# Kernel tuning notes

Hardware: AMD Instinct MI355X
Metric: run time of the kernel (lower is better)

## Reference

```python
import jax, jax.numpy as jnp
import numpy as np

DIM = 1024
HID = 2048
E = 8
K = 2
EPS = 1e-9


def setup_inputs() -> dict:
    key = jax.random.key(0)
    ks = jax.random.split(key, 6)
    scale = 0.02
    return {
        "x": jax.random.normal(ks[0], (4, 2048, DIM), jnp.float32),
        "gate_w": jax.random.normal(ks[1], (DIM, E), jnp.float32) * scale,
        "gate_b": jnp.zeros((E,), jnp.float32),
        # stacked expert weights: leading dim = expert index
        "w1": jax.random.normal(ks[2], (E, DIM, HID), jnp.float32) * scale,
        "b1": jnp.zeros((E, HID), jnp.float32),
        "w2": jax.random.normal(ks[3], (E, DIM, HID), jnp.float32) * scale,
        "b2": jnp.zeros((E, HID), jnp.float32),
        "w3": jax.random.normal(ks[4], (E, HID, DIM), jnp.float32) * scale,
        "b3": jnp.zeros((E, DIM), jnp.float32),
    }


def reference(x, gate_w, gate_b, w1, b1, w2, b2, w3, b3):
    # x: (b, s, d)
    logits = x @ gate_w + gate_b                      # (b, s, E)
    scores = jax.nn.softmax(logits, axis=-1)
    topk_scores, topk_idx = jax.lax.top_k(scores, K)  # (b, s, K)

    usage = scores.mean(axis=(0, 1))                  # (E,)
    load_balance_loss = jnp.sum(usage * jnp.log(usage + EPS))

    # per-expert combine weight: score if expert in top-k else 0  -> (b, s, E)
    onehot = jax.nn.one_hot(topk_idx, E, dtype=x.dtype)            # (b, s, K, E)
    combine = jnp.sum(topk_scores[..., None] * onehot, axis=2)     # (b, s, E)

    out = jnp.zeros_like(x)
    for e in range(E):  # small fixed loop over experts
        gate = jax.nn.sigmoid(x @ w2[e] + b2[e])      # (b, s, H)
        h = (x @ w1[e] + b1[e]) * gate                # SwiGLU hidden
        out = out + combine[..., e:e + 1] * (h @ w3[e] + b3[e])
    return out, load_balance_loss
```

## Files before the change

### kernel.cpp

```cpp
#include <hip/hip_runtime.h>
#include <hip/hip_bf16.h>
#include <math.h>

#define N_TOK 8192
#define DIM   1024
#define HID   2048
#define NE    8
#define NT1   16
#define NT2   32
#define NB1   16
#define NB2   4
#define MAXT  72
#define PANEL1_SH ((size_t)(128 * 256 * 8))
#define PANEL3_SH ((size_t)(256 * 256 * 8))
#define XBLK_SH   ((size_t)(128 * 128 * 8))
#define HBLK_SH   ((size_t)(256 * 128 * 8))

typedef __attribute__((ext_vector_type(8))) short short8;
typedef __attribute__((ext_vector_type(4))) float f32x4;
typedef unsigned short us;

__device__ __forceinline__ us f2bf(float f) {
    unsigned int u = __builtin_bit_cast(unsigned int, f);
    unsigned int r = (u + 0x7fffu + ((u >> 16) & 1u)) >> 16;
    return (us)r;
}
__device__ __forceinline__ float bf2f(us v) {
    unsigned int u = ((unsigned int)v) << 16;
    return __builtin_bit_cast(float, u);
}
__device__ __forceinline__ void gl_lds16(const us* g, us* l) {
    __builtin_amdgcn_global_load_lds(
        (const __attribute__((address_space(1))) void*)g,
        (__attribute__((address_space(3))) void*)l, 16, 0, 0);
}

#define VMW4 asm volatile("s_waitcnt vmcnt(4)" ::: "memory")
#define VMW0 asm volatile("s_waitcnt vmcnt(0)" ::: "memory")
#define BARM asm volatile("s_barrier" ::: "memory")
#define PRIO1 __builtin_amdgcn_s_setprio(1)
#define PRIO0 __builtin_amdgcn_s_setprio(0)

__global__ __launch_bounds__(256) void gate_compute(
    const float* __restrict__ x, const float* __restrict__ gw, const float* __restrict__ gb,
    int* __restrict__ sel, float2* __restrict__ wpair, float* __restrict__ usage_part,
    us* __restrict__ xb)
{
    const int lane = threadIdx.x & 63;
    const int tok = blockIdx.x * 4 + (threadIdx.x >> 6);

    __shared__ float su[NE];
    if (threadIdx.x < NE) su[threadIdx.x] = 0.f;
    __syncthreads();

    float acc[NE];
#pragma unroll
    for (int e = 0; e < NE; e++) acc[e] = 0.f;

    const float* xr = x + (size_t)tok * DIM;
    us* xbr = xb + (size_t)tok * DIM;
    for (int d = lane; d < DIM; d += 64) {
        float xv = xr[d];
        xbr[d] = f2bf(xv);
        const float4* g4 = (const float4*)(gw + (size_t)d * NE);
        float4 ga = g4[0], gc = g4[1];
        acc[0] = fmaf(xv, ga.x, acc[0]);
        acc[1] = fmaf(xv, ga.y, acc[1]);
        acc[2] = fmaf(xv, ga.z, acc[2]);
        acc[3] = fmaf(xv, ga.w, acc[3]);
        acc[4] = fmaf(xv, gc.x, acc[4]);
        acc[5] = fmaf(xv, gc.y, acc[5]);
        acc[6] = fmaf(xv, gc.z, acc[6]);
        acc[7] = fmaf(xv, gc.w, acc[7]);
    }
#pragma unroll
    for (int e = 0; e < NE; e++) {
#pragma unroll
        for (int off = 32; off > 0; off >>= 1)
            acc[e] += __shfl_xor(acc[e], off);
    }

    if (lane == 0) {
        float lg[NE], p[NE];
        float mx = -1e30f;
#pragma unroll
        for (int e = 0; e < NE; e++) { lg[e] = acc[e] + gb[e]; mx = fmaxf(mx, lg[e]); }
        float s = 0.f;
#pragma unroll
        for (int e = 0; e < NE; e++) { p[e] = __expf(lg[e] - mx); s += p[e]; }
        float inv = 1.f / s;
#pragma unroll
        for (int e = 0; e < NE; e++) p[e] *= inv;
#pragma unroll
        for (int e = 0; e < NE; e++) atomicAdd(&su[e], p[e]);

        int e1 = 0; float v1 = p[0];
#pragma unroll
        for (int e = 1; e < NE; e++) if (p[e] > v1) { v1 = p[e]; e1 = e; }
        int e2 = -1; float v2 = -1e30f;
#pragma unroll
        for (int e = 0; e < NE; e++) if (e != e1 && p[e] > v2) { v2 = p[e]; e2 = e; }

        sel[tok] = e1 | (e2 << 4);
        wpair[tok] = make_float2(v1, v2);
    }
    __syncthreads();
    if (threadIdx.x < NE) usage_part[blockIdx.x * NE + threadIdx.x] = su[threadIdx.x];
}

__global__ __launch_bounds__(256) void scan_kernel(
    const int* __restrict__ sel, const float2* __restrict__ wpair,
    int* __restrict__ counts, int* __restrict__ lists, float* __restrict__ wlist)
{
    const int e = blockIdx.x;
    const int t = threadIdx.x;
    const int base_tok = t * 32;

    unsigned selm = 0, km = 0;
#pragma unroll
    for (int i = 0; i < 32; i++) {
        int s = sel[base_tok + i];
        int e1 = s & 15, e2 = (s >> 4) & 15;
        if (e1 == e) selm |= (1u << i);
        else if (e2 == e) { selm |= (1u << i); km |= (1u << i); }
    }
    const int myc = __popc(selm);

    __shared__ int tot[256];
    tot[t] = myc;
    __syncthreads();
#pragma unroll
    for (int d = 1; d < 256; d <<= 1) {
        int v = (t >= d) ? tot[t - d] : 0;
        __syncthreads();
        tot[t] += v;
        __syncthreads();
    }
    int pos = tot[t] - myc;
    if (t == 255) counts[e] = tot[255];

    for (int i = 0; i < 32; i++) {
        if (selm & (1u << i)) {
            int tok = base_tok + i;
            int k = (km >> i) & 1;
            lists[e * N_TOK + pos] = tok * 2 + k;
            float2 wp = wpair[tok];
            wlist[e * N_TOK + pos] = k ? wp.y : wp.x;
            pos++;
        }
    }
}

__global__ __launch_bounds__(256) void usage_reduce(
    const float* __restrict__ part, float* __restrict__ usage)
{
    const int t = threadIdx.x;
    const int e = t & 7, chunk = t >> 3;
    float s = 0.f;
    for (int b = chunk; b < 2048; b += 32) s += part[b * NE + e];
    __shared__ float red[256];
    red[t] = s;
    __syncthreads();
#pragma unroll
    for (int step = 128; step >= 8; step >>= 1) {
        if (t < step) red[t] += red[t + step];
        __syncthreads();
    }
    if (t < NE) usage[t] = red[t];
}

__global__ void loss_kernel(const float* __restrict__ usage, float* __restrict__ out_loss)
{
    if (threadIdx.x == 0) {
        float l = 0.f;
        for (int e = 0; e < NE; e++) {
            float u = usage[e] / (float)N_TOK;
            l += u * logf(u + 1e-9f);
        }
        *out_loss = l;
    }
}

__global__ void prefix_kernel(const int* __restrict__ counts,
                              int* __restrict__ base_exact, int* __restrict__ ntiles,
                              int* __restrict__ tmap_e, int* __restrict__ tmap_m0)
{
    if (threadIdx.x == 0) {
        int bx = 0, nt = 0;
        for (int e = 0; e < NE; e++) {
            base_exact[e] = bx;
            for (int m0 = 0; m0 < counts[e]; m0 += 256) {
                tmap_e[nt] = e; tmap_m0[nt] = m0; nt++;
            }
            bx += counts[e];
        }
        ntiles[0] = nt;
    }
}

__global__ __launch_bounds__(256) void inv_kernel(
    const int* __restrict__ counts, const int* __restrict__ lists,
    const int* __restrict__ base_exact, int* __restrict__ inv)
{
    const int e = blockIdx.y;
    const int idx = blockIdx.x * 256 + threadIdx.x;
    if (idx < counts[e]) inv[lists[e * N_TOK + idx]] = base_exact[e] + idx;
}

__global__ __launch_bounds__(256) void xgather_kernel(
    const us* __restrict__ Xbf,
    const int* __restrict__ counts, const int* __restrict__ lists,
    const int* __restrict__ base_exact,
    us* __restrict__ Xg)
{
    __shared__ int toks[128];
    __shared__ int bexs[NE], cnts[NE];
    const int t = threadIdx.x;
    if (t < NE) { bexs[t] = base_exact[t]; cnts[t] = counts[t]; }
    __syncthreads();
    if (t < 128) {
        int gpos = blockIdx.x * 128 + t;
        int e = 0;
#pragma unroll
        for (int k = 1; k < NE; k++) if (gpos >= bexs[k]) e = k;
        int idx = gpos - bexs[e];
        int tok = (idx < cnts[e]) ? (lists[e * N_TOK + idx] >> 1) : 0;
        toks[t] = tok;
    }
    __syncthreads();

    us* op = Xg + (size_t)blockIdx.x * XBLK_SH;
    const int rr = t & 127;
    const int ch = t >> 7;
    const us* srcrow = Xbf + (size_t)toks[rr] * DIM;
#pragma unroll
    for (int it = 0; it < 64; it++) {
        int c = it * 2 + ch;
        short8 v = *(const short8*)(srcrow + c * 8);
        *(short8*)(op + (size_t)(c * 128 + rr) * 8) = v;
    }
}

__global__ __launch_bounds__(256) void wswz12_kernel(
    const float* __restrict__ w1, const float* __restrict__ w2, us* __restrict__ out)
{
    const int e = blockIdx.z, nbx = blockIdx.y, gs = blockIdx.x;
    us* op = out + ((size_t)e * NB1 + nbx) * PANEL1_SH + (size_t)gs * 8 * 256 * 8;
    const float* w1e = w1 + (size_t)e * DIM * HID;
    const float* w2e = w2 + (size_t)e * DIM * HID;
    const int t = threadIdx.x;
#pragma unroll
    for (int it = 0; it < 8; it++) {
        int idx = it * 256 + t;
        int g = idx >> 8, row = idx & 255;
        int col = nbx * 128 + (row & 127);
        const float* src = (row < 128 ? w1e : w2e) + (size_t)((gs * 8 + g) * 8) * HID + col;
        short8 v;
#pragma unroll
        for (int s = 0; s < 8; s++) v[s] = (short)f2bf(src[(size_t)s * HID]);
        *(short8*)(op + (size_t)idx * 8) = v;
    }
}

__global__ __launch_bounds__(256) void wswz3_kernel(
    const float* __restrict__ w3, us* __restrict__ out)
{
    const int e = blockIdx.z, nbx = blockIdx.y, gs = blockIdx.x;
    us* op = out + ((size_t)e * NB2 + nbx) * PANEL3_SH + (size_t)gs * 8 * 256 * 8;
    const float* w3e = w3 + (size_t)e * HID * DIM;
    const int t = threadIdx.x;
#pragma unroll
    for (int it = 0; it < 8; it++) {
        int idx = it * 256 + t;
        int g = idx >> 8, row = idx & 255;
        int col = nbx * 256 + row;
        const float* src = w3e + (size_t)((gs * 8 + g) * 8) * DIM + col;
        short8 v;
#pragma unroll
        for (int s = 0; s < 8; s++) v[s] = (short)f2bf(src[(size_t)s * DIM]);
        *(short8*)(op + (size_t)idx * 8) = v;
    }
}

#define ABUF(b) ((us*)(SM + (b)*32768))
#define BBUF(b) ((us*)(SM + 65536 + (b)*32768))

#define AF_READ(b, h) do {                                               \
    _Pragma("unroll")                                                    \
    for (int mi = 0; mi < 8; mi++)                                       \
        af[mi] = *(const short8*)(ABUF(b) + ((h)*1024 + kc*256 + Mw + mi*16 + fr)*8); \
} while (0)
#define BF_READ4(b, h) do {                                              \
    _Pragma("unroll")                                                    \
    for (int j = 0; j < 4; j++)                                          \
        bfv[j] = *(const short8*)(BBUF(b) + ((h)*1024 + kc*256 + Nw + j*16 + fr)*8); \
} while (0)
#define CLUST4 do {                                                      \
    PRIO1;                                                               \
    _Pragma("unroll")                                                    \
    for (int j = 0; j < 4; j++) {                                        \
        _Pragma("unroll")                                                \
        for (int mi = 0; mi < 8; mi++)                                   \
            acc[mi][j] = __builtin_amdgcn_mfma_f32_16x16x32_bf16(        \
                af[mi], bfv[j], acc[mi][j], 0, 0, 0);                    \
    }                                                                    \
    PRIO0;                                                               \
} while (0)

__global__ __launch_bounds__(512, 2) void ffn1_mfma_kernel(
    const us* __restrict__ Xg, const us* __restrict__ W12sw,
    const float* __restrict__ b1, const float* __restrict__ b2,
    const int* __restrict__ counts, const int* __restrict__ base_exact,
    const int* __restrict__ ntiles, const int* __restrict__ tmap_e, const int* __restrict__ tmap_m0,
    us* __restrict__ Hsw)
{
    const int hw = blockIdx.x;
    const int ix = hw >> 3;
    const int nbx = ((hw & 7) << 1) | (ix & 1);
    const int by  = ix >> 1;
    if (by >= ntiles[0]) return;
    const int e  = tmap_e[by];
    const int m0 = tmap_m0[by];
    const int cnt = counts[e];
    const int bex = base_exact[e];

    __shared__ __align__(16) unsigned char SM[132096];

    const int t = threadIdx.x;
    const int lane = t & 63, wv = t >> 6;
    const int wr = wv >> 2, wc = wv & 3;
    const int Mw = wr * 128, Nw = wc * 64;
    const int fr = lane & 15, kc = lane >> 4;

    float bb[4];
    {
        const float* bsrc = (wc < 2) ? b1 : b2;
#pragma unroll
        for (int ni = 0; ni < 4; ni++)
            bb[ni] = bsrc[e * HID + nbx * 128 + (wc & 1) * 64 + ni * 16 + fr];
    }
    __syncthreads();

    const int c0 = wv * 128 + lane;
    const int c1 = c0 + 64;
    const int RA0 = min(bex + m0 + (c0 & 255), N_TOK * 2 - 1);
    const int RA1 = min(bex + m0 + (c1 & 255), N_TOK * 2 - 1);
    const us* ApA = Xg + (size_t)(RA0 >> 7) * XBLK_SH + (size_t)(c0 >> 8) * 1024 + (RA0 & 127) * 8;
    const us* ApB = Xg + (size_t)(RA1 >> 7) * XBLK_SH + (size_t)(c1 >> 8) * 1024 + (RA1 & 127) * 8;
    const us* Wp = W12sw + ((size_t)e * NB1 + nbx) * PANEL1_SH;
    const int dbase = wv * 128 * 8;

    f32x4 acc[8][4];
    const f32x4 fz = {0.f, 0.f, 0.f, 0.f};
#pragma unroll
    for (int i = 0; i < 8; i++)
#pragma unroll
        for (int j = 0; j < 4; j++) acc[i][j] = fz;

    #define STAGE_A(b, tile, h) do {                                             \
        gl_lds16(ApA + (size_t)((tile)*8 + (h)*4) * 1024, ABUF(b) + ((h)*1024)*8 + dbase); \
        gl_lds16(ApB + (size_t)((tile)*8 + (h)*4) * 1024, ABUF(b) + ((h)*1024 + 64)*8 + dbase); \
    } while (0)
    #define STAGE_B(b, tile, h) do {                                             \
        const us* s_ = Wp + ((size_t)(tile)*2048 + (h)*1024) * 8;                \
        gl_lds16(s_ + (size_t)c0 * 8, BBUF(b) + ((h)*1024)*8 + dbase);           \
        gl_lds16(s_ + (size_t)c1 * 8, BBUF(b) + ((h)*1024 + 64)*8 + dbase);      \
    } while (0)

    short8 af[8], bfv[4];

    STAGE_A(0, 0, 0); STAGE_B(0, 0, 0); STAGE_A(0, 0, 1); STAGE_B(0, 0, 1);
    VMW4; BARM;

    for (int tl = 0; tl < NT1; ++tl) {
        const int b = tl & 1, nb = b ^ 1;
        const bool more = (tl + 1 < NT1);
        AF_READ(b, 0); BF_READ4(b, 0);
        if (more) { STAGE_A(nb, tl + 1, 0); STAGE_B(nb, tl + 1, 0); VMW4; } else { VMW0; }
        BARM; CLUST4; BARM;
        AF_READ(b, 1); BF_READ4(b, 1);
        if (more) { STAGE_A(nb, tl + 1, 1); STAGE_B(nb, tl + 1, 1); VMW4; }
        BARM; CLUST4; BARM;
    }
    #undef STAGE_A
    #undef STAGE_B

    float* G = (float*)SM;
    if (wc >= 2) {
        const int cp = wc - 2;
#pragma unroll
        for (int ni = 0; ni < 4; ni++) {
            int c2 = cp * 64 + ni * 16 + fr;
#pragma unroll
            for (int mi = 0; mi < 8; mi++) {
#pragma unroll
                for (int j = 0; j < 4; j++) {
                    int m = mi * 16 + kc * 4 + j;
                    float g = 1.f / (1.f + __expf(-(acc[mi][ni][j] + bb[ni])));
                    G[(wr * 128 + c2) * 129 + m] = g;
                }
            }
        }
    }
    __syncthreads();
    if (wc < 2) {
#pragma unroll
        for (int ni = 0; ni < 4; ni++) {
            int c2 = wc * 64 + ni * 16 + fr;
            int ch = nbx * 128 + c2;
            size_t cb = (size_t)(ch >> 3) * 128 * 8 + (ch & 7);
#pragma unroll
            for (int mi = 0; mi < 8; mi++) {
#pragma unroll
                for (int j = 0; j < 4; j++) {
                    int m = mi * 16 + kc * 4 + j;
                    int rl = wr * 128 + m;
                    if (m0 + rl >= cnt) continue;
                    float h = (acc[mi][ni][j] + bb[ni]) * G[(wr * 128 + c2) * 129 + m];
                    int R = bex + m0 + rl;
                    Hsw[(size_t)(R >> 7) * HBLK_SH + cb + (size_t)(R & 127) * 8] = f2bf(h);
                }
            }
        }
    }
}

__global__ __launch_bounds__(512, 2) void ffn2_mfma_kernel(
    const us* __restrict__ Hsw, const us* __restrict__ W3sw, const float* __restrict__ b3,
    const int* __restrict__ counts, const int* __restrict__ base_exact,
    const int* __restrict__ ntiles, const int* __restrict__ tmap_e, const int* __restrict__ tmap_m0,
    const float* __restrict__ wts,
    us* __restrict__ Pb)
{
    const int hw = blockIdx.x;
    const int xcd = hw & 7;
    const int ix = hw >> 3;
    const int nbx = xcd & 3;
    const int by = (ix << 1) | (xcd >> 2);
    if (by >= ntiles[0]) return;
    const int e  = tmap_e[by];
    const int m0 = tmap_m0[by];
    const int cnt = counts[e];
    const int bex = base_exact[e];

    __shared__ __align__(16) unsigned char SM[132096];
    float* rowwt = (float*)(SM + 131072);

    const int t = threadIdx.x;
    if (t < 256) {
        int idx = m0 + t;
        rowwt[t] = (idx < cnt) ? wts[e * N_TOK + idx] : 0.f;
    }

    const int lane = t & 63, wv = t >> 6;
    const int wr = wv >> 2, wc = wv & 3;
    const int Mw = wr * 128, Nw = wc * 64;
    const int fr = lane & 15, kc = lane >> 4;

    float bb3[4];
#pragma unroll
    for (int ni = 0; ni < 4; ni++)
        bb3[ni] = b3[e * DIM + nbx * 256 + wc * 64 + ni * 16 + fr];
    __syncthreads();

    const int c0 = wv * 128 + lane;
    const int c1 = c0 + 64;
    const int RA0 = min(bex + m0 + (c0 & 255), N_TOK * 2 - 1);
    const int RA1 = min(bex + m0 + (c1 & 255), N_TOK * 2 - 1);
    const us* HpA = Hsw + (size_t)(RA0 >> 7) * HBLK_SH + (size_t)(c0 >> 8) * 1024 + (RA0 & 127) * 8;
    const us* HpB = Hsw + (size_t)(RA1 >> 7) * HBLK_SH + (size_t)(c1 >> 8) * 1024 + (RA1 & 127) * 8;
    const us* Wp = W3sw + ((size_t)e * NB2 + nbx) * PANEL3_SH;
    const int dbase = wv * 128 * 8;

    f32x4 acc[8][4];
    const f32x4 fz = {0.f, 0.f, 0.f, 0.f};
#pragma unroll
    for (int i = 0; i < 8; i++)
#pragma unroll
        for (int j = 0; j < 4; j++) acc[i][j] = fz;

    #define STAGE_A2(b, tile, h) do {                                            \
        gl_lds16(HpA + (size_t)((tile)*8 + (h)*4) * 1024, ABUF(b) + ((h)*1024)*8 + dbase); \
        gl_lds16(HpB + (size_t)((tile)*8 + (h)*4) * 1024, ABUF(b) + ((h)*1024 + 64)*8 + dbase); \
    } while (0)
    #define STAGE_B2(b, tile, h) do {                                            \
        const us* s_ = Wp + ((size_t)(tile)*2048 + (h)*1024) * 8;                \
        gl_lds16(s_ + (size_t)c0 * 8, BBUF(b) + ((h)*1024)*8 + dbase);           \
        gl_lds16(s_ + (size_t)c1 * 8, BBUF(b) + ((h)*1024 + 64)*8 + dbase);      \
    } while (0)

    short8 af[8], bfv[4];

    STAGE_A2(0, 0, 0); STAGE_B2(0, 0, 0); STAGE_A2(0, 0, 1); STAGE_B2(0, 0, 1);
    VMW4; BARM;

    for (int tl = 0; tl < NT2; ++tl) {
        const int b = tl & 1, nb = b ^ 1;
        const bool more = (tl + 1 < NT2);
        AF_READ(b, 0); BF_READ4(b, 0);
        if (more) { STAGE_A2(nb, tl + 1, 0); STAGE_B2(nb, tl + 1, 0); VMW4; } else { VMW0; }
        BARM; CLUST4; BARM;
        AF_READ(b, 1); BF_READ4(b, 1);
        if (more) { STAGE_A2(nb, tl + 1, 1); STAGE_B2(nb, tl + 1, 1); VMW4; }
        BARM; CLUST4; BARM;
    }
    #undef STAGE_A2
    #undef STAGE_B2

#pragma unroll
    for (int ni = 0; ni < 4; ni++) {
        int col = nbx * 256 + wc * 64 + ni * 16 + fr;
#pragma unroll
        for (int mi = 0; mi < 8; mi++) {
#pragma unroll
            for (int j = 0; j < 4; j++) {
                int rl = wr * 128 + mi * 16 + kc * 4 + j;
                if (m0 + rl >= cnt) continue;
                float v = (acc[mi][ni][j] + bb3[ni]) * rowwt[rl];
                Pb[(size_t)(bex + m0 + rl) * DIM + col] = f2bf(v);
            }
        }
    }
}

__global__ __launch_bounds__(256) void combine_kernel(
    const us* __restrict__ Pb, const int* __restrict__ inv,
    float* __restrict__ out)
{
    int gid = blockIdx.x * 256 + threadIdx.x;
    int tok = gid >> 7;
    int c8 = (gid & 127) * 8;
    const short8 a = *(const short8*)(Pb + (size_t)inv[tok * 2] * DIM + c8);
    const short8 b = *(const short8*)(Pb + (size_t)inv[tok * 2 + 1] * DIM + c8);
    float4 r0, r1;
    r0.x = bf2f((us)a[0]) + bf2f((us)b[0]);
    r0.y = bf2f((us)a[1]) + bf2f((us)b[1]);
    r0.z = bf2f((us)a[2]) + bf2f((us)b[2]);
    r0.w = bf2f((us)a[3]) + bf2f((us)b[3]);
    r1.x = bf2f((us)a[4]) + bf2f((us)b[4]);
    r1.y = bf2f((us)a[5]) + bf2f((us)b[5]);
    r1.z = bf2f((us)a[6]) + bf2f((us)b[6]);
    r1.w = bf2f((us)a[7]) + bf2f((us)b[7]);
    float* o = out + (size_t)tok * DIM + c8;
    *(float4*)o = r0;
    *(float4*)(o + 4) = r1;
}

extern "C" void kernel_launch(void* const* d_in, const int* in_sizes, int n_in,
                              void* d_out, int out_size, void* d_ws, size_t ws_size,
                              hipStream_t stream) {
    (void)in_sizes; (void)n_in; (void)out_size; (void)ws_size;
    const float* x      = (const float*)d_in[0];
    const float* gate_w = (const float*)d_in[1];
    const float* gate_b = (const float*)d_in[2];
    const float* w1     = (const float*)d_in[3];
    const float* b1     = (const float*)d_in[4];
    const float* w2     = (const float*)d_in[5];
    const float* b2     = (const float*)d_in[6];
    const float* w3     = (const float*)d_in[7];
    const float* b3     = (const float*)d_in[8];
    float* out = (float*)d_out;

    char* ws = (char*)d_ws;
    float* usage      = (float*)ws;
    int*   counts     = (int*)(ws + 32);
    int*   base_exact = (int*)(ws + 64);
    int*   ntiles     = (int*)(ws + 96);
    int*   tmap_e     = (int*)(ws + 128);
    int*   tmap_m0    = (int*)(ws + 640);
    int*   lists      = (int*)(ws + 4096);
    float* wts        = (float*)(ws + 4096 + (size_t)NE * N_TOK * 4);
    int*   inv        = (int*)(ws + 4096 + (size_t)2 * NE * N_TOK * 4);
    int*   sel        = (int*)(ws + 4096 + 576 * 1024);
    float2* wpair     = (float2*)(ws + 4096 + 608 * 1024);
    float* usage_part = (float*)(ws + 4096 + 672 * 1024);
    us* Hsw   = (us*)(ws + (1ull  << 20));
    us* W12sw = (us*)(ws + (65ull << 20));
    us* W3sw  = W12sw;
    us* Pb    = (us*)(ws + (97ull << 20));
    us* Xbf   = (us*)(ws + (65ull << 20));
    us* Xg    = (us*)d_out;

    gate_compute<<<N_TOK / 4, 256, 0, stream>>>(x, gate_w, gate_b, sel, wpair, usage_part, Xbf);
    scan_kernel<<<NE, 256, 0, stream>>>(sel, wpair, counts, lists, wts);
    usage_reduce<<<1, 256, 0, stream>>>(usage_part, usage);
    prefix_kernel<<<1, 64, 0, stream>>>(counts, base_exact, ntiles, tmap_e, tmap_m0);
    {
        dim3 gI(N_TOK / 256, NE);
        inv_kernel<<<gI, 256, 0, stream>>>(counts, lists, base_exact, inv);
    }
    xgather_kernel<<<N_TOK * 2 / 128, 256, 0, stream>>>(Xbf, counts, lists, base_exact, Xg);

    dim3 gW12(16, NB1, NE);
    wswz12_kernel<<<gW12, 256, 0, stream>>>(w1, w2, W12sw);

    ffn1_mfma_kernel<<<NB1 * MAXT, 512, 0, stream>>>(Xg, W12sw, b1, b2, counts, base_exact,
                                                     ntiles, tmap_e, tmap_m0, Hsw);

    loss_kernel<<<1, 64, 0, stream>>>(usage, out + (size_t)N_TOK * DIM);

    dim3 gW3(32, NB2, NE);
    wswz3_kernel<<<gW3, 256, 0, stream>>>(w3, W3sw);

    ffn2_mfma_kernel<<<4 * MAXT, 512, 0, stream>>>(Hsw, W3sw, b3, counts, base_exact,
                                                   ntiles, tmap_e, tmap_m0, wts, Pb);
    combine_kernel<<<N_TOK * 128 / 256, 256, 0, stream>>>(Pb, inv, out);
}
```

Baseline: 492.1 us.

## Switch FFN GEMM mainloops to 4-stage LDS ring with 3-deep prefetch

Replaces the double-buffered half-tile pipeline in both expert GEMM kernels with a 4-slot ring of 32-wide K-slices, keeping three slices of global-to-LDS loads in flight. The staging address layout is simplified to one row pointer per thread with coalesced weight loads. The aim is to hide global memory latency better behind MFMA work. The cost is a deeper vmcnt accounting scheme and tail handling that must be exactly right, and the LDS footprint stays at the same 128KB.

```diff
diff --git a/kernel.cpp b/kernel.cpp
--- a/kernel.cpp
+++ b/kernel.cpp
@@ -6,8 +6,8 @@
 #define DIM   1024
 #define HID   2048
 #define NE    8
-#define NT1   16
-#define NT2   32
+#define NKS1  32
+#define NKS2  64
 #define NB1   16
 #define NB2   4
 #define MAXT  72
@@ -35,6 +35,7 @@
         (__attribute__((address_space(3))) void*)l, 16, 0, 0);
 }
 
+#define VMW8 asm volatile("s_waitcnt vmcnt(8)" ::: "memory")
 #define VMW4 asm volatile("s_waitcnt vmcnt(4)" ::: "memory")
 #define VMW0 asm volatile("s_waitcnt vmcnt(0)" ::: "memory")
 #define BARM asm volatile("s_barrier" ::: "memory")
@@ -282,20 +283,10 @@
     }
 }
 
-#define ABUF(b) ((us*)(SM + (b)*32768))
-#define BBUF(b) ((us*)(SM + 65536 + (b)*32768))
-
-#define AF_READ(b, h) do {                                               \
-    _Pragma("unroll")                                                    \
-    for (int mi = 0; mi < 8; mi++)                                       \
-        af[mi] = *(const short8*)(ABUF(b) + ((h)*1024 + kc*256 + Mw + mi*16 + fr)*8); \
-} while (0)
-#define BF_READ4(b, h) do {                                              \
-    _Pragma("unroll")                                                    \
-    for (int j = 0; j < 4; j++)                                          \
-        bfv[j] = *(const short8*)(BBUF(b) + ((h)*1024 + kc*256 + Nw + j*16 + fr)*8); \
-} while (0)
-#define CLUST4 do {                                                      \
+#define SA(s) ((us*)(SM + (s)*32768))
+#define SB(s) ((us*)(SM + (s)*32768 + 16384))
+
+#define CLUST32 do {                                                     \
     PRIO1;                                                               \
     _Pragma("unroll")                                                    \
     for (int j = 0; j < 4; j++) {                                        \
@@ -307,6 +298,15 @@
     PRIO0;                                                               \
 } while (0)
 
+#define FRAG_READ(s) do {                                                \
+    _Pragma("unroll")                                                    \
+    for (int mi = 0; mi < 8; mi++)                                       \
+        af[mi] = *(const short8*)(SA(s) + (kc*256 + Mw + mi*16 + fr)*8); \
+    _Pragma("unroll")                                                    \
+    for (int j = 0; j < 4; j++)                                          \
+        bfv[j] = *(const short8*)(SB(s) + (kc*256 + Nw + j*16 + fr)*8);  \
+} while (0)
+
 __global__ __launch_bounds__(512, 2) void ffn1_mfma_kernel(
     const us* __restrict__ Xg, const us* __restrict__ W12sw,
     const float* __restrict__ b1, const float* __restrict__ b2,
@@ -341,14 +341,21 @@
     }
     __syncthreads();
 
-    const int c0 = wv * 128 + lane;
-    const int c1 = c0 + 64;
-    const int RA0 = min(bex + m0 + (c0 & 255), N_TOK * 2 - 1);
-    const int RA1 = min(bex + m0 + (c1 & 255), N_TOK * 2 - 1);
-    const us* ApA = Xg + (size_t)(RA0 >> 7) * XBLK_SH + (size_t)(c0 >> 8) * 1024 + (RA0 & 127) * 8;
-    const us* ApB = Xg + (size_t)(RA1 >> 7) * XBLK_SH + (size_t)(c1 >> 8) * 1024 + (RA1 & 127) * 8;
-    const us* Wp = W12sw + ((size_t)e * NB1 + nbx) * PANEL1_SH;
-    const int dbase = wv * 128 * 8;
+    const int arow = t & 255;
+    const int kq0  = t >> 8;
+    const int RA = min(bex + m0 + arow, N_TOK * 2 - 1);
+    const us* ApR = Xg + (size_t)(RA >> 7) * XBLK_SH + (RA & 127) * 8;
+    const us* Wp  = W12sw + ((size_t)e * NB1 + nbx) * PANEL1_SH;
+    const int db0 = (t & ~63) * 8;
+    const int db1 = db0 + 512 * 8;
+
+    #define F1_STAGE(ks) do {                                                   \
+        const int s_ = (ks) & 3;                                                \
+        gl_lds16(ApR + (size_t)((ks)*4 + kq0)     * 1024, SA(s_) + db0);        \
+        gl_lds16(ApR + (size_t)((ks)*4 + kq0 + 2) * 1024, SA(s_) + db1);        \
+        gl_lds16(Wp + ((size_t)(ks)*1024 + t)       * 8,  SB(s_) + db0);        \
+        gl_lds16(Wp + ((size_t)(ks)*1024 + t + 512) * 8,  SB(s_) + db1);        \
+    } while (0)
 
     f32x4 acc[8][4];
     const f32x4 fz = {0.f, 0.f, 0.f, 0.f};
@@ -357,33 +364,21 @@
 #pragma unroll
         for (int j = 0; j < 4; j++) acc[i][j] = fz;
 
-    #define STAGE_A(b, tile, h) do {                                             \
-        gl_lds16(ApA + (size_t)((tile)*8 + (h)*4) * 1024, ABUF(b) + ((h)*1024)*8 + dbase); \
-        gl_lds16(ApB + (size_t)((tile)*8 + (h)*4) * 1024, ABUF(b) + ((h)*1024 + 64)*8 + dbase); \
-    } while (0)
-    #define STAGE_B(b, tile, h) do {                                             \
-        const us* s_ = Wp + ((size_t)(tile)*2048 + (h)*1024) * 8;                \
-        gl_lds16(s_ + (size_t)c0 * 8, BBUF(b) + ((h)*1024)*8 + dbase);           \
-        gl_lds16(s_ + (size_t)c1 * 8, BBUF(b) + ((h)*1024 + 64)*8 + dbase);      \
-    } while (0)
-
     short8 af[8], bfv[4];
 
-    STAGE_A(0, 0, 0); STAGE_B(0, 0, 0); STAGE_A(0, 0, 1); STAGE_B(0, 0, 1);
-    VMW4; BARM;
-
-    for (int tl = 0; tl < NT1; ++tl) {
-        const int b = tl & 1, nb = b ^ 1;
-        const bool more = (tl + 1 < NT1);
-        AF_READ(b, 0); BF_READ4(b, 0);
-        if (more) { STAGE_A(nb, tl + 1, 0); STAGE_B(nb, tl + 1, 0); VMW4; } else { VMW0; }
-        BARM; CLUST4; BARM;
-        AF_READ(b, 1); BF_READ4(b, 1);
-        if (more) { STAGE_A(nb, tl + 1, 1); STAGE_B(nb, tl + 1, 1); VMW4; }
-        BARM; CLUST4; BARM;
-    }
-    #undef STAGE_A
-    #undef STAGE_B
+    F1_STAGE(0); F1_STAGE(1); F1_STAGE(2);
+    VMW8; BARM;
+
+    for (int ks = 0; ks < NKS1; ++ks) {
+        FRAG_READ(ks & 3);
+        if (ks + 3 < NKS1)      { F1_STAGE(ks + 3); VMW8; }
+        else if (ks == NKS1 - 3) { VMW4; }
+        else if (ks == NKS1 - 2) { VMW0; }
+        BARM;
+        CLUST32;
+        BARM;
+    }
+    #undef F1_STAGE
 
     float* G = (float*)SM;
     if (wc >= 2) {
@@ -463,14 +458,21 @@
         bb3[ni] = b3[e * DIM + nbx * 256 + wc * 64 + ni * 16 + fr];
     __syncthreads();
 
-    const int c0 = wv * 128 + lane;
-    const int c1 = c0 + 64;
-    const int RA0 = min(bex + m0 + (c0 & 255), N_TOK * 2 - 1);
-    const int RA1 = min(bex + m0 + (c1 & 255), N_TOK * 2 - 1);
-    const us* HpA = Hsw + (size_t)(RA0 >> 7) * HBLK_SH + (size_t)(c0 >> 8) * 1024 + (RA0 & 127) * 8;
-    const us* HpB = Hsw + (size_t)(RA1 >> 7) * HBLK_SH + (size_t)(c1 >> 8) * 1024 + (RA1 & 127) * 8;
-    const us* Wp = W3sw + ((size_t)e * NB2 + nbx) * PANEL3_SH;
-    const int dbase = wv * 128 * 8;
+    const int arow = t & 255;
+    const int kq0  = t >> 8;
+    const int RA = min(bex + m0 + arow, N_TOK * 2 - 1);
+    const us* HpR = Hsw + (size_t)(RA >> 7) * HBLK_SH + (RA & 127) * 8;
+    const us* Wp  = W3sw + ((size_t)e * NB2 + nbx) * PANEL3_SH;
+    const int db0 = (t & ~63) * 8;
+    const int db1 = db0 + 512 * 8;
+
+    #define F2_STAGE(ks) do {                                                   \
+        const int s_ = (ks) & 3;                                                \
+        gl_lds16(HpR + (size_t)((ks)*4 + kq0)     * 1024, SA(s_) + db0);        \
+        gl_lds16(HpR + (size_t)((ks)*4 + kq0 + 2) * 1024, SA(s_) + db1);        \
+        gl_lds16(Wp + ((size_t)(ks)*1024 + t)       * 8,  SB(s_) + db0);        \
+        gl_lds16(Wp + ((size_t)(ks)*1024 + t + 512) * 8,  SB(s_) + db1);        \
+    } while (0)
 
     f32x4 acc[8][4];
     const f32x4 fz = {0.f, 0.f, 0.f, 0.f};
@@ -479,33 +481,21 @@
 #pragma unroll
         for (int j = 0; j < 4; j++) acc[i][j] = fz;
 
-    #define STAGE_A2(b, tile, h) do {                                            \
-        gl_lds16(HpA + (size_t)((tile)*8 + (h)*4) * 1024, ABUF(b) + ((h)*1024)*8 + dbase); \
-        gl_lds16(HpB + (size_t)((tile)*8 + (h)*4) * 1024, ABUF(b) + ((h)*1024 + 64)*8 + dbase); \
-    } while (0)
-    #define STAGE_B2(b, tile, h) do {                                            \
-        const us* s_ = Wp + ((size_t)(tile)*2048 + (h)*1024) * 8;                \
-        gl_lds16(s_ + (size_t)c0 * 8, BBUF(b) + ((h)*1024)*8 + dbase);           \
-        gl_lds16(s_ + (size_t)c1 * 8, BBUF(b) + ((h)*1024 + 64)*8 + dbase);      \
-    } while (0)
-
     short8 af[8], bfv[4];
 
-    STAGE_A2(0, 0, 0); STAGE_B2(0, 0, 0); STAGE_A2(0, 0, 1); STAGE_B2(0, 0, 1);
-    VMW4; BARM;
-
-    for (int tl = 0; tl < NT2; ++tl) {
-        const int b = tl & 1, nb = b ^ 1;
-        const bool more = (tl + 1 < NT2);
-        AF_READ(b, 0); BF_READ4(b, 0);
-        if (more) { STAGE_A2(nb, tl + 1, 0); STAGE_B2(nb, tl + 1, 0); VMW4; } else { VMW0; }
-        BARM; CLUST4; BARM;
-        AF_READ(b, 1); BF_READ4(b, 1);
-        if (more) { STAGE_A2(nb, tl + 1, 1); STAGE_B2(nb, tl + 1, 1); VMW4; }
-        BARM; CLUST4; BARM;
-    }
-    #undef STAGE_A2
-    #undef STAGE_B2
+    F2_STAGE(0); F2_STAGE(1); F2_STAGE(2);
+    VMW8; BARM;
+
+    for (int ks = 0; ks < NKS2; ++ks) {
+        FRAG_READ(ks & 3);
+        if (ks + 3 < NKS2)      { F2_STAGE(ks + 3); VMW8; }
+        else if (ks == NKS2 - 3) { VMW4; }
+        else if (ks == NKS2 - 2) { VMW0; }
+        BARM;
+        CLUST32;
+        BARM;
+    }
+    #undef F2_STAGE
 
 #pragma unroll
     for (int ni = 0; ni < 4; ni++) {
```

Result: no change. 494.8 us (+0.5%).
